# Performance work log

Hardware: AMD Instinct MI355X
Metric: run time of the kernel (lower is better)

The kernel has to match this reference:

```python
import jax, jax.numpy as jnp
import numpy as np

NUM_CLASSES = 100000
NUM_SAMPLED = 5000  # num_classes * cr, cr = 0.05
BATCH = 4096
DIM = 1024


def _log_expected_count(idx, num_sampled, num_classes):
    # TF LogUniformCandidateSampler: P(c) = log((c+2)/(c+1)) / log(num_classes+1)
    c = idx.astype(jnp.float32)
    p = jnp.log((c + 2.0) / (c + 1.0)) / jnp.log(float(num_classes) + 1.0)
    # expected count for unique sampling of num_sampled candidates
    return jnp.log(-jnp.expm1(num_sampled * jnp.log1p(-p)))


def setup_inputs() -> dict:
    key = jax.random.key(0)
    k1, k2, k3, k4 = jax.random.split(key, 4)
    x = jax.random.normal(k1, (BATCH, DIM), dtype=jnp.float32)
    w = jax.random.normal(k2, (DIM, NUM_CLASSES), dtype=jnp.float32) * 0.05  # tf random_normal_initializer stddev
    b = jnp.zeros((NUM_CLASSES,), dtype=jnp.float32)
    labels = jax.random.randint(k3, (BATCH,), 0, NUM_CLASSES)
    sampled = jax.random.randint(k4, (NUM_SAMPLED,), 0, NUM_CLASSES)
    return {"x": x, "w": w, "b": b, "labels": labels, "sampled": sampled}


def reference(x, w, b, labels, sampled):
    # sampled-class logits: gather columns of w then one small GEMM
    w_s = w[:, sampled]                                   # [D, S]
    sampled_logits = x @ w_s + b[sampled][None, :]        # [B, S]
    sampled_logits = sampled_logits - _log_expected_count(sampled, NUM_SAMPLED, NUM_CLASSES)[None, :]
    # true-class logit per example
    w_t = w[:, labels]                                    # [D, B]
    true_logits = jnp.einsum('bd,db->b', x, w_t) + b[labels]
    true_logits = true_logits - _log_expected_count(labels, NUM_SAMPLED, NUM_CLASSES)
    # softmax CE with true class in column 0 of [true | sampled]
    all_logits = jnp.concatenate([true_logits[:, None], sampled_logits], axis=1)  # [B, 1+S]
    loss = jnp.mean(jax.nn.logsumexp(all_logits, axis=1) - true_logits)
    return loss
```

## Files before the change

### kernel.cpp

```cpp
#include <hip/hip_runtime.h>
#include <hip/hip_bf16.h>

#define NUM_CLASSES 100000
#define NUM_SAMPLED 5000
#define BATCH 4096
#define DIM 1024
#define NPAD 5120

typedef float floatx4 __attribute__((ext_vector_type(4)));
typedef short bf16x8 __attribute__((ext_vector_type(8)));

__device__ __forceinline__ float log_expected_count(int c) {
    float p = log1pf(1.0f / (float)(c + 1)) / logf((float)NUM_CLASSES + 1.0f);
    float t = (float)NUM_SAMPLED * log1pf(-p);
    return logf(-expm1f(t));
}

__device__ __forceinline__ void async_ld16(const void* g, void* l) {
    __builtin_amdgcn_global_load_lds(
        (const __attribute__((address_space(1))) unsigned int*)g,
        (__attribute__((address_space(3))) unsigned int*)l,
        16, 0, 0);
}

__global__ __launch_bounds__(256) void init_kernel(float* rowsum) {
    int i = blockIdx.x * 256 + threadIdx.x;
    if (i < BATCH) rowsum[i] = 0.0f;
}

__global__ __launch_bounds__(256) void convert_x_kernel(const float* __restrict__ x,
                                                        __hip_bfloat16* __restrict__ A) {
    int i = (blockIdx.x * 256 + threadIdx.x) * 4;
    float4 v = *reinterpret_cast<const float4*>(x + i);
    union { ushort4 u; __hip_bfloat16 h[4]; } o;
    o.h[0] = __float2bfloat16(v.x);
    o.h[1] = __float2bfloat16(v.y);
    o.h[2] = __float2bfloat16(v.z);
    o.h[3] = __float2bfloat16(v.w);
    *reinterpret_cast<ushort4*>(A + i) = o.u;
}

__global__ __launch_bounds__(256) void gather_b_kernel(const float* __restrict__ w,
                                                       const float* __restrict__ b,
                                                       const int* __restrict__ sampled,
                                                       __hip_bfloat16* __restrict__ BT,
                                                       float* __restrict__ shift) {
    int n  = blockIdx.x * 256 + threadIdx.x;
    int k0 = blockIdx.y * 16;
    bool valid = (n < NUM_SAMPLED);
    int c = valid ? sampled[n] : 0;
    if (blockIdx.y == 0) {
        shift[n] = valid ? (b[c] - log_expected_count(c)) : -1e30f;
    }
    __hip_bfloat16* dst = BT + (size_t)n * DIM + k0;
    if (valid) {
        const float* src = w + (size_t)k0 * NUM_CLASSES + c;
        #pragma unroll
        for (int kk = 0; kk < 16; kk += 8) {
            union { uint4 u; __hip_bfloat16 h[8]; } o;
            #pragma unroll
            for (int j = 0; j < 8; j++)
                o.h[j] = __float2bfloat16(src[(size_t)(kk + j) * NUM_CLASSES]);
            *reinterpret_cast<uint4*>(dst + kk) = o.u;
        }
    } else {
        uint4 z; z.x = z.y = z.z = z.w = 0u;
        #pragma unroll
        for (int kk = 0; kk < 16; kk += 8)
            *reinterpret_cast<uint4*>(dst + kk) = z;
    }
}

#define BM 128
#define BN 128
#define BK 64

__global__ __launch_bounds__(256) void gemm_kernel(const __hip_bfloat16* __restrict__ A,
                                                   const __hip_bfloat16* __restrict__ BT,
                                                   const float* __restrict__ shift,
                                                   float* __restrict__ rowsum) {
    __shared__ __hip_bfloat16 As[BM * BK];
    __shared__ __hip_bfloat16 Bs[BN * BK];

    const int tid  = threadIdx.x;
    const int m0   = blockIdx.x * BM;
    const int n0   = blockIdx.y * BN;
    const int lane = tid & 63;
    const int wv   = tid >> 6;
    const int wm   = (wv >> 1) * 64;
    const int wn   = (wv & 1) * 64;
    const int col  = lane & 15;
    const int quad = lane >> 4;

    floatx4 acc[4][4] = {};

    const __hip_bfloat16* gA[4];
    const __hip_bfloat16* gB[4];
    int ldsOff[4];
    #pragma unroll
    for (int r = 0; r < 4; r++) {
        int eo  = tid * 8 + r * 2048;
        int row = eo >> 6;
        int cl  = eo & 63;
        gA[r] = A  + (size_t)(m0 + row) * DIM + cl;
        gB[r] = BT + (size_t)(n0 + row) * DIM + cl;
        ldsOff[r] = eo;
    }

    for (int kt = 0; kt < DIM; kt += BK) {
        #pragma unroll
        for (int r = 0; r < 4; r++)
            async_ld16(gA[r] + kt, &As[ldsOff[r]]);
        #pragma unroll
        for (int r = 0; r < 4; r++)
            async_ld16(gB[r] + kt, &Bs[ldsOff[r]]);
        __syncthreads();

        #pragma unroll
        for (int ks = 0; ks < 2; ks++) {
            const int kc = ks * 32 + quad * 8;
            bf16x8 af[4], bfr[4];
            #pragma unroll
            for (int i = 0; i < 4; i++) {
                af[i]  = *reinterpret_cast<const bf16x8*>(&As[(wm + i * 16 + col) * BK + kc]);
                bfr[i] = *reinterpret_cast<const bf16x8*>(&Bs[(wn + i * 16 + col) * BK + kc]);
            }
            #pragma unroll
            for (int i = 0; i < 4; i++)
                #pragma unroll
                for (int j = 0; j < 4; j++)
                    acc[i][j] = __builtin_amdgcn_mfma_f32_16x16x32_bf16(af[i], bfr[j], acc[i][j], 0, 0, 0);
        }
        __syncthreads();
    }

    float sh[4];
    #pragma unroll
    for (int j = 0; j < 4; j++)
        sh[j] = shift[n0 + wn + j * 16 + col];

    #pragma unroll
    for (int i = 0; i < 4; i++) {
        #pragma unroll
        for (int r = 0; r < 4; r++) {
            float s = 0.0f;
            #pragma unroll
            for (int j = 0; j < 4; j++)
                s += __expf(acc[i][j][r] + sh[j]);
            s += __shfl_xor(s, 1);
            s += __shfl_xor(s, 2);
            s += __shfl_xor(s, 4);
            s += __shfl_xor(s, 8);
            if (col == 0) {
                int mrow = m0 + wm + i * 16 + quad * 4 + r;
                atomicAdd(&rowsum[mrow], s);
            }
        }
    }
}

__global__ __launch_bounds__(256) void rowloss_kernel(const float* __restrict__ x,
                                                      const float* __restrict__ w,
                                                      const float* __restrict__ b,
                                                      const int* __restrict__ labels,
                                                      const float* __restrict__ rowsum,
                                                      float* __restrict__ rowloss) {
    __shared__ float red[4];
    const int m = blockIdx.x;
    const int t = threadIdx.x;
    const int lbl = labels[m];
    const float* xr = x + (size_t)m * DIM;
    const float* wc = w + lbl;

    float p = 0.0f;
    #pragma unroll
    for (int d = t; d < DIM; d += 256)
        p += xr[d] * wc[(size_t)d * NUM_CLASSES];

    #pragma unroll
    for (int off = 32; off > 0; off >>= 1)
        p += __shfl_xor(p, off);
    if ((t & 63) == 0) red[t >> 6] = p;
    __syncthreads();
    if (t == 0) {
        float tl = red[0] + red[1] + red[2] + red[3] + b[lbl] - log_expected_count(lbl);
        float total = rowsum[m] + __expf(tl);
        rowloss[m] = logf(total) - tl;
    }
}

__global__ __launch_bounds__(256) void reduce_kernel(const float* __restrict__ rowloss,
                                                     float* __restrict__ out) {
    __shared__ float red[4];
    const int t = threadIdx.x;
    float s = 0.0f;
    #pragma unroll
    for (int i = t; i < BATCH; i += 256)
        s += rowloss[i];
    #pragma unroll
    for (int off = 32; off > 0; off >>= 1)
        s += __shfl_xor(s, off);
    if ((t & 63) == 0) red[t >> 6] = s;
    __syncthreads();
    if (t == 0)
        out[0] = (red[0] + red[1] + red[2] + red[3]) * (1.0f / (float)BATCH);
}

extern "C" void kernel_launch(void* const* d_in, const int* in_sizes, int n_in,
                              void* d_out, int out_size, void* d_ws, size_t ws_size,
                              hipStream_t stream) {
    const float* x       = (const float*)d_in[0];
    const float* w       = (const float*)d_in[1];
    const float* b       = (const float*)d_in[2];
    const int*   labels  = (const int*)d_in[3];
    const int*   sampled = (const int*)d_in[4];
    float* out = (float*)d_out;

    char* ws = (char*)d_ws;
    __hip_bfloat16* A  = (__hip_bfloat16*)(ws);
    __hip_bfloat16* BT = (__hip_bfloat16*)(ws + (size_t)8  * 1024 * 1024);
    float* shift   = (float*)(ws + (size_t)18 * 1024 * 1024);
    float* rowsum  = (float*)(ws + (size_t)18 * 1024 * 1024 + 64 * 1024);
    float* rowloss = (float*)(ws + (size_t)18 * 1024 * 1024 + 128 * 1024);

    hipLaunchKernelGGL(init_kernel, dim3(16), dim3(256), 0, stream, rowsum);
    hipLaunchKernelGGL(convert_x_kernel, dim3((BATCH * DIM / 4) / 256), dim3(256), 0, stream, x, A);
    hipLaunchKernelGGL(gather_b_kernel, dim3(NPAD / 256, DIM / 16), dim3(256), 0, stream,
                       w, b, sampled, BT, shift);
    hipLaunchKernelGGL(gemm_kernel, dim3(BATCH / BM, NPAD / BN), dim3(256), 0, stream,
                       A, BT, shift, rowsum);
    hipLaunchKernelGGL(rowloss_kernel, dim3(BATCH), dim3(256), 0, stream,
                       x, w, b, labels, rowsum, rowloss);
    hipLaunchKernelGGL(reduce_kernel, dim3(1), dim3(256), 0, stream, rowloss, out);
}
```

Before: 719.3 us.

## Gather sampled and label columns of w via cache-line buckets in one pass

Sampled and label class indices are bucketed by 64-byte cache line of w (16 classes per line) using atomic counters. An extract kernel then reads each touched line once per row d and scatters the values into the bf16 B matrix and a new fp32 label-weight matrix WT. The rowloss kernel now reads WT contiguously with float4 loads, one wavefront per row, instead of doing strided column reads of w. This replaces scattered, uncoalesced column gathers with line-level reads. It risks dropping entries silently if a line gets more than SLACK hits, and the scattered writes to BT and WT are strided by DIM.

```diff
diff --git a/kernel.cpp b/kernel.cpp
--- a/kernel.cpp
+++ b/kernel.cpp
@@ -6,6 +6,8 @@
 #define BATCH 4096
 #define DIM 1024
 #define NPAD 5120
+#define NLINES 6250
+#define SLACK 32
 
 typedef float floatx4 __attribute__((ext_vector_type(4)));
 typedef short bf16x8 __attribute__((ext_vector_type(8)));
@@ -23,9 +25,16 @@
         16, 0, 0);
 }
 
-__global__ __launch_bounds__(256) void init_kernel(float* rowsum) {
+__global__ __launch_bounds__(256) void setup_kernel(int* __restrict__ cnt,
+                                                    float* __restrict__ rowsum,
+                                                    uint4* __restrict__ btpad) {
     int i = blockIdx.x * 256 + threadIdx.x;
+    if (i < NLINES) cnt[i] = 0;
     if (i < BATCH) rowsum[i] = 0.0f;
+    if (i < (NPAD - NUM_SAMPLED) * DIM * 2 / 16) {
+        uint4 z; z.x = z.y = z.z = z.w = 0u;
+        btpad[i] = z;
+    }
 }
 
 __global__ __launch_bounds__(256) void convert_x_kernel(const float* __restrict__ x,
@@ -40,34 +49,50 @@
     *reinterpret_cast<ushort4*>(A + i) = o.u;
 }
 
-__global__ __launch_bounds__(256) void gather_b_kernel(const float* __restrict__ w,
-                                                       const float* __restrict__ b,
-                                                       const int* __restrict__ sampled,
-                                                       __hip_bfloat16* __restrict__ BT,
-                                                       float* __restrict__ shift) {
-    int n  = blockIdx.x * 256 + threadIdx.x;
-    int k0 = blockIdx.y * 16;
-    bool valid = (n < NUM_SAMPLED);
-    int c = valid ? sampled[n] : 0;
-    if (blockIdx.y == 0) {
-        shift[n] = valid ? (b[c] - log_expected_count(c)) : -1e30f;
-    }
-    __hip_bfloat16* dst = BT + (size_t)n * DIM + k0;
-    if (valid) {
-        const float* src = w + (size_t)k0 * NUM_CLASSES + c;
-        #pragma unroll
-        for (int kk = 0; kk < 16; kk += 8) {
-            union { uint4 u; __hip_bfloat16 h[8]; } o;
-            #pragma unroll
-            for (int j = 0; j < 8; j++)
-                o.h[j] = __float2bfloat16(src[(size_t)(kk + j) * NUM_CLASSES]);
-            *reinterpret_cast<uint4*>(dst + kk) = o.u;
-        }
-    } else {
-        uint4 z; z.x = z.y = z.z = z.w = 0u;
-        #pragma unroll
-        for (int kk = 0; kk < 16; kk += 8)
-            *reinterpret_cast<uint4*>(dst + kk) = z;
+__global__ __launch_bounds__(256) void bucket_kernel(const int* __restrict__ sampled,
+                                                     const int* __restrict__ labels,
+                                                     const float* __restrict__ b,
+                                                     int* __restrict__ cnt,
+                                                     unsigned* __restrict__ entries,
+                                                     float* __restrict__ shift,
+                                                     float* __restrict__ tlshift) {
+    int t = blockIdx.x * 256 + threadIdx.x;
+    if (t < NUM_SAMPLED) {
+        int c = sampled[t];
+        int pos = atomicAdd(&cnt[c >> 4], 1);
+        if (pos < SLACK)
+            entries[(c >> 4) * SLACK + pos] = ((unsigned)(c & 15) << 28) | (unsigned)t;
+        shift[t] = b[c] - log_expected_count(c);
+    } else if (t < NPAD) {
+        shift[t] = -1e30f;
+    } else if (t < NPAD + BATCH) {
+        int m = t - NPAD;
+        int c = labels[m];
+        int pos = atomicAdd(&cnt[c >> 4], 1);
+        if (pos < SLACK)
+            entries[(c >> 4) * SLACK + pos] = ((unsigned)(c & 15) << 28) | (1u << 27) | (unsigned)m;
+        tlshift[m] = b[c] - log_expected_count(c);
+    }
+}
+
+__global__ __launch_bounds__(256) void extract_kernel(const float* __restrict__ w,
+                                                      const int* __restrict__ cnt,
+                                                      const unsigned* __restrict__ entries,
+                                                      __hip_bfloat16* __restrict__ BT,
+                                                      float* __restrict__ WT) {
+    int line = blockIdx.x * 256 + threadIdx.x;
+    int d = blockIdx.y;
+    if (line >= NLINES) return;
+    int c = cnt[line];
+    if (c == 0) return;
+    if (c > SLACK) c = SLACK;
+    const float* src = w + (size_t)d * NUM_CLASSES + line * 16;
+    for (int e = 0; e < c; e++) {
+        unsigned E = entries[line * SLACK + e];
+        float v = src[E >> 28];
+        unsigned idx = E & 0x3FFFu;
+        if (E & (1u << 27)) WT[(size_t)idx * DIM + d] = v;
+        else                BT[(size_t)idx * DIM + d] = __float2bfloat16(v);
     }
 }
 
@@ -160,30 +185,26 @@
 }
 
 __global__ __launch_bounds__(256) void rowloss_kernel(const float* __restrict__ x,
-                                                      const float* __restrict__ w,
-                                                      const float* __restrict__ b,
-                                                      const int* __restrict__ labels,
+                                                      const float* __restrict__ WT,
+                                                      const float* __restrict__ tlshift,
                                                       const float* __restrict__ rowsum,
                                                       float* __restrict__ rowloss) {
-    __shared__ float red[4];
-    const int m = blockIdx.x;
-    const int t = threadIdx.x;
-    const int lbl = labels[m];
-    const float* xr = x + (size_t)m * DIM;
-    const float* wc = w + lbl;
-
+    int m = blockIdx.x * 4 + (threadIdx.x >> 6);
+    int lane = threadIdx.x & 63;
+    const float4* xr = reinterpret_cast<const float4*>(x + (size_t)m * DIM);
+    const float4* wr = reinterpret_cast<const float4*>(WT + (size_t)m * DIM);
     float p = 0.0f;
     #pragma unroll
-    for (int d = t; d < DIM; d += 256)
-        p += xr[d] * wc[(size_t)d * NUM_CLASSES];
-
+    for (int j = 0; j < 4; j++) {
+        float4 a = xr[lane + 64 * j];
+        float4 b = wr[lane + 64 * j];
+        p += a.x * b.x + a.y * b.y + a.z * b.z + a.w * b.w;
+    }
     #pragma unroll
     for (int off = 32; off > 0; off >>= 1)
         p += __shfl_xor(p, off);
-    if ((t & 63) == 0) red[t >> 6] = p;
-    __syncthreads();
-    if (t == 0) {
-        float tl = red[0] + red[1] + red[2] + red[3] + b[lbl] - log_expected_count(lbl);
+    if (lane == 0) {
+        float tl = p + tlshift[m];
         float total = rowsum[m] + __expf(tl);
         rowloss[m] = logf(total) - tl;
     }
@@ -219,17 +240,24 @@
     char* ws = (char*)d_ws;
     __hip_bfloat16* A  = (__hip_bfloat16*)(ws);
     __hip_bfloat16* BT = (__hip_bfloat16*)(ws + (size_t)8  * 1024 * 1024);
-    float* shift   = (float*)(ws + (size_t)18 * 1024 * 1024);
-    float* rowsum  = (float*)(ws + (size_t)18 * 1024 * 1024 + 64 * 1024);
-    float* rowloss = (float*)(ws + (size_t)18 * 1024 * 1024 + 128 * 1024);
-
-    hipLaunchKernelGGL(init_kernel, dim3(16), dim3(256), 0, stream, rowsum);
+    float* WT      = (float*)(ws + (size_t)18 * 1024 * 1024);
+    float* shift   = (float*)(ws + (size_t)34 * 1024 * 1024);
+    float* tlshift = (float*)(ws + (size_t)34 * 1024 * 1024 + 64  * 1024);
+    float* rowsum  = (float*)(ws + (size_t)34 * 1024 * 1024 + 128 * 1024);
+    float* rowloss = (float*)(ws + (size_t)34 * 1024 * 1024 + 192 * 1024);
+    int* cnt       = (int*)  (ws + (size_t)34 * 1024 * 1024 + 256 * 1024);
+    unsigned* ent  = (unsigned*)(ws + (size_t)34 * 1024 * 1024 + 320 * 1024);
+
+    hipLaunchKernelGGL(setup_kernel, dim3(64), dim3(256), 0, stream,
+                       cnt, rowsum, (uint4*)(BT + (size_t)NUM_SAMPLED * DIM));
     hipLaunchKernelGGL(convert_x_kernel, dim3((BATCH * DIM / 4) / 256), dim3(256), 0, stream, x, A);
-    hipLaunchKernelGGL(gather_b_kernel, dim3(NPAD / 256, DIM / 16), dim3(256), 0, stream,
-                       w, b, sampled, BT, shift);
+    hipLaunchKernelGGL(bucket_kernel, dim3((NPAD + BATCH) / 256), dim3(256), 0, stream,
+                       sampled, labels, b, cnt, ent, shift, tlshift);
+    hipLaunchKernelGGL(extract_kernel, dim3((NLINES + 255) / 256, DIM), dim3(256), 0, stream,
+                       w, cnt, ent, BT, WT);
     hipLaunchKernelGGL(gemm_kernel, dim3(BATCH / BM, NPAD / BN), dim3(256), 0, stream,
                        A, BT, shift, rowsum);
-    hipLaunchKernelGGL(rowloss_kernel, dim3(BATCH), dim3(256), 0, stream,
-                       x, w, b, labels, rowsum, rowloss);
+    hipLaunchKernelGGL(rowloss_kernel, dim3(BATCH / 4), dim3(256), 0, stream,
+                       x, WT, tlshift, rowsum, rowloss);
     hipLaunchKernelGGL(reduce_kernel, dim3(1), dim3(256), 0, stream, rowloss, out);
 }
```

After: 735.3 us. 2.2% more time.
